# Kernel tuning notes

Hardware: AMD Instinct MI355X
Metric: run time of the kernel (lower is better)

## Reference

```python
import jax, jax.numpy as jnp
import numpy as np

EMBED_DIM = 128
HIDDEN_DIM = 512
NUM_LAYERS = 2
LATENT_DIM = 128
VOCAB = 2048
BATCH = 4096
NEG = -1.0e9  # matches torch masked fill value -1e9
TEMPERATURE = 1.0  # generate() skips the divide when temperature == 1.0


def _gru_cell(x, h, w_ih, w_hh, b_ih, b_hh):
    # PyTorch GRU cell, gate order (r, z, n)
    gi = x @ w_ih.T + b_ih          # [B, 3H]
    gh = h @ w_hh.T + b_hh          # [B, 3H]
    i_r, i_z, i_n = jnp.split(gi, 3, axis=-1)
    h_r, h_z, h_n = jnp.split(gh, 3, axis=-1)
    r = jax.nn.sigmoid(i_r + h_r)
    u = jax.nn.sigmoid(i_z + h_z)
    n = jnp.tanh(i_n + r * h_n)
    return (1.0 - u) * n + u * h


def setup_inputs() -> dict:
    key = jax.random.key(0)
    ks = jax.random.split(key, 16)

    def unif(k, shape, fan):
        bound = 1.0 / np.sqrt(fan)
        return jax.random.uniform(k, shape, jnp.float32, -bound, bound)

    embed = jax.random.normal(ks[0], (VOCAB, EMBED_DIM), jnp.float32)
    embed = embed.at[0].set(0.0)  # padding_idx = 0

    return dict(
        z=jax.random.normal(ks[1], (BATCH, LATENT_DIM), jnp.float32),
        embed=embed,
        w_lh=unif(ks[2], (NUM_LAYERS * HIDDEN_DIM, LATENT_DIM), LATENT_DIM),
        b_lh=unif(ks[3], (NUM_LAYERS * HIDDEN_DIM,), LATENT_DIM),
        w_ih0=unif(ks[4], (3 * HIDDEN_DIM, EMBED_DIM), HIDDEN_DIM),
        w_hh0=unif(ks[5], (3 * HIDDEN_DIM, HIDDEN_DIM), HIDDEN_DIM),
        b_ih0=unif(ks[6], (3 * HIDDEN_DIM,), HIDDEN_DIM),
        b_hh0=unif(ks[7], (3 * HIDDEN_DIM,), HIDDEN_DIM),
        w_ih1=unif(ks[8], (3 * HIDDEN_DIM, HIDDEN_DIM), HIDDEN_DIM),
        w_hh1=unif(ks[9], (3 * HIDDEN_DIM, HIDDEN_DIM), HIDDEN_DIM),
        b_ih1=unif(ks[10], (3 * HIDDEN_DIM,), HIDDEN_DIM),
        b_hh1=unif(ks[11], (3 * HIDDEN_DIM,), HIDDEN_DIM),
        w_out=unif(ks[12], (VOCAB, HIDDEN_DIM), HIDDEN_DIM),
        b_out=unif(ks[13], (VOCAB,), HIDDEN_DIM),
        bos_idx=1, eos_idx=2, pad_idx=0,
        max_len=64, top_k=40, min_generation_length=20,
    )


def reference(z, embed, w_lh, b_lh, w_ih0, w_hh0, b_ih0, b_hh0,
              w_ih1, w_hh1, b_ih1, b_hh1, w_out, b_out,
              bos_idx, eos_idx, pad_idx, max_len, top_k, min_generation_length):
    B = z.shape[0]
    V = w_out.shape[0]
    H = w_hh0.shape[1]
    eff_min = max(0, min(int(min_generation_length), max(0, max_len - 2)))

    # latent -> initial hidden state [L, B, H]
    h = jnp.tanh(z @ w_lh.T + b_lh).reshape(B, NUM_LAYERS, H).transpose(1, 0, 2)
    rows = jnp.arange(B)[:, None]

    def step(carry, t):
        h, cur, finished, key = carry
        key, sk = jax.random.split(key)
        x = embed[cur]                                   # [B, E]
        h0 = _gru_cell(x, h[0], w_ih0, w_hh0, b_ih0, b_hh0)
        h1 = _gru_cell(h0, h[1], w_ih1, w_hh1, b_ih1, b_hh1)
        logits = h1 @ w_out.T + b_out                    # [B, V]
        logits = logits.at[:, bos_idx].set(NEG).at[:, pad_idx].set(NEG)
        # block EOS until min_generation_length real tokens emitted
        logits = jnp.where((t - 1) < eff_min, logits.at[:, eos_idx].set(NEG), logits)
        if TEMPERATURE != 1.0:
            logits = logits / max(TEMPERATURE, 1e-6)
        if 0 < top_k < V:
            tv, ti = jax.lax.top_k(logits, top_k)
            logits = jnp.full_like(logits, NEG).at[rows, ti].set(tv)
        # multinomial over softmax(logits) == categorical on logits
        nxt = jax.random.categorical(sk, logits).astype(jnp.int32)
        nxt = jnp.where(finished, pad_idx, nxt)
        finished = finished | (nxt == eos_idx)
        return (jnp.stack([h0, h1]), nxt, finished, key), nxt

    init = (h,
            jnp.full((B,), bos_idx, jnp.int32),
            jnp.zeros((B,), dtype=bool),
            jax.random.key(1))
    _, toks = jax.lax.scan(step, init, jnp.arange(1, max_len))  # toks: [max_len-1, B]
    return jnp.concatenate(
        [jnp.full((B, 1), bos_idx, jnp.int32), toks.T.astype(jnp.int32)], axis=1)
```

## Files before the change

kernel.cpp:

```cpp
#include <hip/hip_runtime.h>
#include <cstdint>
#include <cstddef>

#ifndef PARTITIONABLE
#define PARTITIONABLE 1
#endif

namespace {
constexpr int kBatch  = 4096;
constexpr int kEmb    = 128;
constexpr int kHid    = 512;
constexpr int kVoc    = 2048;
constexpr int kMaxLen = 64;
constexpr int kTopK   = 40;
constexpr int kBos = 1, kEos = 2, kPad = 0;
constexpr int kEffMin = 20;
constexpr float kNeg  = -1.0e9f;
constexpr float kTiny = 1.17549435082228751e-38f;
}

typedef __bf16 bf16x8 __attribute__((ext_vector_type(8)));
typedef float  f32x4  __attribute__((ext_vector_type(4)));

__host__ __device__ inline void tf2x32(uint32_t k0, uint32_t k1,
                                       uint32_t x0, uint32_t x1,
                                       uint32_t& o0, uint32_t& o1) {
  uint32_t ks0 = k0, ks1 = k1, ks2 = k0 ^ k1 ^ 0x1BD11BDAu;
  x0 += ks0; x1 += ks1;
#define TFR(r) { x0 += x1; x1 = (x1 << (r)) | (x1 >> (32 - (r))); x1 ^= x0; }
  TFR(13) TFR(15) TFR(26) TFR(6)   x0 += ks1; x1 += ks2 + 1u;
  TFR(17) TFR(29) TFR(16) TFR(24)  x0 += ks2; x1 += ks0 + 2u;
  TFR(13) TFR(15) TFR(26) TFR(6)   x0 += ks0; x1 += ks1 + 3u;
  TFR(17) TFR(29) TFR(16) TFR(24)  x0 += ks1; x1 += ks2 + 4u;
  TFR(13) TFR(15) TFR(26) TFR(6)   x0 += ks2; x1 += ks0 + 5u;
#undef TFR
  o0 = x0; o1 = x1;
}

__device__ __forceinline__ float xla_tanh(float x) {
  float ax = fabsf(x);
  float xc = fminf(fmaxf(x, -9.0f), 9.0f);
  float x2 = __fmul_rn(xc, xc);
  float num = -2.76076847742355e-16f;
  num = __fadd_rn(__fmul_rn(x2, num), 2.00018790482477e-13f);
  num = __fadd_rn(__fmul_rn(x2, num), -8.60467152213735e-11f);
  num = __fadd_rn(__fmul_rn(x2, num), 5.12229709037114e-08f);
  num = __fadd_rn(__fmul_rn(x2, num), 1.48572235717979e-05f);
  num = __fadd_rn(__fmul_rn(x2, num), 6.37261928875436e-04f);
  num = __fadd_rn(__fmul_rn(x2, num), 4.89352455891786e-03f);
  num = __fmul_rn(xc, num);
  float den = 1.19825839466702e-06f;
  den = __fadd_rn(__fmul_rn(x2, den), 1.18534705686654e-04f);
  den = __fadd_rn(__fmul_rn(x2, den), 2.26843463243900e-03f);
  den = __fadd_rn(__fmul_rn(x2, den), 4.89352518554385e-03f);
  return (ax < 4.0e-04f) ? x : __fdiv_rn(num, den);
}

__device__ __forceinline__ float xla_sigmoid(float x) {
  return __fdiv_rn(1.0f, __fadd_rn(1.0f, expf(-x)));
}

__device__ __forceinline__ void gl_lds16(const void* g, void* l) {
  __builtin_amdgcn_global_load_lds(
      (const __attribute__((address_space(1))) void*)g,
      (__attribute__((address_space(3))) void*)l, 16, 0, 0);
}

__device__ __forceinline__ void split3(float a, __bf16& a0, __bf16& a1, __bf16& a2) {
  a0 = (__bf16)a;
  float r1 = __fsub_rn(a, (float)a0);
  a1 = (__bf16)r1;
  float r2 = __fsub_rn(r1, (float)a1);
  a2 = (__bf16)r2;
}

template <int ACT>
__global__ __launch_bounds__(256) void gemm2(
    const float* __restrict__ A0, const float* __restrict__ B0,
    const float* __restrict__ bias0, float* __restrict__ C0,
    const float* __restrict__ A1, const float* __restrict__ B1,
    const float* __restrict__ bias1, float* __restrict__ C1,
    int lda, int ldb, int ldc, int K) {
  __shared__ __attribute__((aligned(16))) float As[2][128 * 16];
  __shared__ __attribute__((aligned(16))) float Bs[2][16 * 128];

  const float* A    = blockIdx.z ? A1 : A0;
  const float* Bt   = blockIdx.z ? B1 : B0;
  const float* bias = blockIdx.z ? bias1 : bias0;
  float*       C    = blockIdx.z ? C1 : C0;

  const int tid = threadIdx.x;
  const int w = tid >> 6, l = tid & 63;
  const int bm = blockIdx.y * 128;
  const int bn = blockIdx.x * 128;
  const int tx = tid & 15, ty = tid >> 4;
  const int t3 = ty & 3;

  const int arow  = w * 16 + (l >> 2);
  const int agran = (l & 3) ^ ((l >> 2) & 3);
  const float* pA = A + (size_t)(bm + arow) * lda + agran * 4;
  const int bk = w * 2 + (l >> 5);
  const int bnc = (l & 31) * 4;
  const float* pB = Bt + (size_t)bk * ldb + bn + bnc;

  float acc[8][8];
#pragma unroll
  for (int i = 0; i < 8; ++i)
#pragma unroll
    for (int j = 0; j < 8; ++j) acc[i][j] = 0.0f;

  const int nt = K >> 4;
  gl_lds16(pA,            &As[0][w * 256]);
  gl_lds16(pA + 64 * lda, &As[0][(4 + w) * 256]);
  gl_lds16(pB,            &Bs[0][w * 256]);
  gl_lds16(pB + (size_t)8 * ldb, &Bs[0][(4 + w) * 256]);
  __syncthreads();

  for (int t = 0; t < nt; ++t) {
    const int cur = t & 1;
    if (t + 1 < nt) {
      const float* qA = pA + (t + 1) * 16;
      const float* qB = pB + (size_t)(t + 1) * 16 * ldb;
      gl_lds16(qA,            &As[cur ^ 1][w * 256]);
      gl_lds16(qA + 64 * lda, &As[cur ^ 1][(4 + w) * 256]);
      gl_lds16(qB,            &Bs[cur ^ 1][w * 256]);
      gl_lds16(qB + (size_t)8 * ldb, &Bs[cur ^ 1][(4 + w) * 256]);
    }
    const float* as = As[cur];
    const float* bs = Bs[cur];
#pragma unroll
    for (int g = 0; g < 4; ++g) {
      float4 bv0[4], bv1[4];
#pragma unroll
      for (int q = 0; q < 4; ++q) {
        bv0[q] = *(const float4*)&bs[(g * 4 + q) * 128 + tx * 4];
        bv1[q] = *(const float4*)&bs[(g * 4 + q) * 128 + 64 + tx * 4];
      }
#pragma unroll
      for (int ii = 0; ii < 8; ++ii) {
        float4 a = *(const float4*)&as[(ty + 16 * ii) * 16 + ((g ^ t3) * 4)];
        float ak[4] = {a.x, a.y, a.z, a.w};
#pragma unroll
        for (int q = 0; q < 4; ++q) {
          const float av_ = ak[q];
          const float4 b0 = bv0[q], b1 = bv1[q];
          acc[ii][0] += av_ * b0.x; acc[ii][1] += av_ * b0.y;
          acc[ii][2] += av_ * b0.z; acc[ii][3] += av_ * b0.w;
          acc[ii][4] += av_ * b1.x; acc[ii][5] += av_ * b1.y;
          acc[ii][6] += av_ * b1.z; acc[ii][7] += av_ * b1.w;
        }
      }
    }
    __syncthreads();
  }

  const int c0 = bn + tx * 4, c1 = bn + 64 + tx * 4;
  const float4 bs0 = *(const float4*)&bias[c0];
  const float4 bs1 = *(const float4*)&bias[c1];
#pragma unroll
  for (int ii = 0; ii < 8; ++ii) {
    const int r = bm + ty + 16 * ii;
    float4 o0, o1;
    o0.x = acc[ii][0] + bs0.x; o0.y = acc[ii][1] + bs0.y;
    o0.z = acc[ii][2] + bs0.z; o0.w = acc[ii][3] + bs0.w;
    o1.x = acc[ii][4] + bs1.x; o1.y = acc[ii][5] + bs1.y;
    o1.z = acc[ii][6] + bs1.z; o1.w = acc[ii][7] + bs1.w;
    if (ACT == 1) {
      o0.x = xla_tanh(o0.x); o0.y = xla_tanh(o0.y);
      o0.z = xla_tanh(o0.z); o0.w = xla_tanh(o0.w);
      o1.x = xla_tanh(o1.x); o1.y = xla_tanh(o1.y);
      o1.z = xla_tanh(o1.z); o1.w = xla_tanh(o1.w);
    }
    *(float4*)(C + (size_t)r * ldc + c0) = o0;
    *(float4*)(C + (size_t)r * ldc + c1) = o1;
  }
}

struct GemmArgs {
  const __bf16 *a0, *a1, *a2;
  const __bf16 *b0, *b1, *b2;
  const float* bias;
  float* c;
};

__global__ __launch_bounds__(256, 3) void gemm_mx3(
    GemmArgs g0, GemmArgs g1, int N) {
  __shared__ __attribute__((aligned(16))) __bf16 lds[6 * 4096];

  const GemmArgs g = blockIdx.z ? g1 : g0;
  const int tid = threadIdx.x;
  const int nwg = gridDim.x * gridDim.y;
  const int lin = blockIdx.y * gridDim.x + blockIdx.x;
  const int swz = (lin & 7) * (nwg >> 3) + (lin >> 3);
  const int bm = (swz / gridDim.x) * 128;
  const int bn = (swz % gridDim.x) * 128;
  const int lane = tid & 63;
  const int w  = tid >> 6;
  const int wm = w & 1;
  const int wn = w >> 1;
  const int l15 = lane & 15;
  const int kge = (lane >> 4) * 8;

  const int srow = tid >> 2;
  const int sge  = (tid & 3) * 8;
  const __bf16* tp[6];
  tp[0] = g.a0 + (size_t)(bm + srow) * 512 + sge;
  tp[1] = g.a1 + (size_t)(bm + srow) * 512 + sge;
  tp[2] = g.a2 + (size_t)(bm + srow) * 512 + sge;
  tp[3] = g.b0 + (size_t)(bn + srow) * 512 + sge;
  tp[4] = g.b1 + (size_t)(bn + srow) * 512 + sge;
  tp[5] = g.b2 + (size_t)(bn + srow) * 512 + sge;

  int aoff[4], boff[4];
#pragma unroll
  for (int i = 0; i < 4; ++i) {
    aoff[i] = (wm * 64 + i * 16 + l15) * 32 + kge;
    boff[i] = (wn * 64 + i * 16 + l15) * 32 + kge;
  }

  f32x4 acc[4][4] = {};

  for (int s = 0; s < 16; ++s) {
    const int k0 = s * 32;
#pragma unroll
    for (int p = 0; p < 6; ++p) {
      gl_lds16(tp[p] + k0,                    &lds[p * 4096 + w * 512]);
      gl_lds16(tp[p] + (size_t)64 * 512 + k0, &lds[p * 4096 + 2048 + w * 512]);
    }
    __syncthreads();

    bf16x8 Af[3][4];
#pragma unroll
    for (int mi = 0; mi < 4; ++mi) {
      Af[0][mi] = *(const bf16x8*)&lds[0 * 4096 + aoff[mi]];
      Af[1][mi] = *(const bf16x8*)&lds[1 * 4096 + aoff[mi]];
      Af[2][mi] = *(const bf16x8*)&lds[2 * 4096 + aoff[mi]];
    }
#pragma unroll
    for (int nj = 0; nj < 4; ++nj) {
      bf16x8 B0 = *(const bf16x8*)&lds[3 * 4096 + boff[nj]];
      bf16x8 B1 = *(const bf16x8*)&lds[4 * 4096 + boff[nj]];
      bf16x8 B2 = *(const bf16x8*)&lds[5 * 4096 + boff[nj]];
#pragma unroll
      for (int mi = 0; mi < 4; ++mi) {
        f32x4 c = acc[mi][nj];
        c = __builtin_amdgcn_mfma_f32_16x16x32_bf16(Af[2][mi], B2, c, 0, 0, 0);
        c = __builtin_amdgcn_mfma_f32_16x16x32_bf16(Af[2][mi], B1, c, 0, 0, 0);
        c = __builtin_amdgcn_mfma_f32_16x16x32_bf16(Af[1][mi], B2, c, 0, 0, 0);
        c = __builtin_amdgcn_mfma_f32_16x16x32_bf16(Af[2][mi], B0, c, 0, 0, 0);
        c = __builtin_amdgcn_mfma_f32_16x16x32_bf16(Af[1][mi], B1, c, 0, 0, 0);
        c = __builtin_amdgcn_mfma_f32_16x16x32_bf16(Af[0][mi], B2, c, 0, 0, 0);
        c = __builtin_amdgcn_mfma_f32_16x16x32_bf16(Af[1][mi], B0, c, 0, 0, 0);
        c = __builtin_amdgcn_mfma_f32_16x16x32_bf16(Af[0][mi], B1, c, 0, 0, 0);
        c = __builtin_amdgcn_mfma_f32_16x16x32_bf16(Af[0][mi], B0, c, 0, 0, 0);
        acc[mi][nj] = c;
      }
    }
    __syncthreads();
  }

#pragma unroll
  for (int mi = 0; mi < 4; ++mi) {
    const int row0 = bm + wm * 64 + mi * 16 + (lane >> 4) * 4;
#pragma unroll
    for (int nj = 0; nj < 4; ++nj) {
      const int col = bn + wn * 64 + nj * 16 + l15;
      const float bv = g.bias[col];
      f32x4 v = acc[mi][nj];
#pragma unroll
      for (int r = 0; r < 4; ++r)
        g.c[(size_t)(row0 + r) * N + col] = v[r] + bv;
    }
  }
}

__global__ __launch_bounds__(256, 2) void gemm_gru0(
    const __bf16* __restrict__ a0, const __bf16* __restrict__ a1,
    const __bf16* __restrict__ a2,
    const __bf16* __restrict__ wb0, const __bf16* __restrict__ wb1,
    const __bf16* __restrict__ wb2,
    const float* __restrict__ bias, const float* __restrict__ Eih0,
    const int* __restrict__ curTok,
    __bf16* __restrict__ q0, __bf16* __restrict__ q1,
    __bf16* __restrict__ q2) {
  __shared__ __attribute__((aligned(16))) __bf16 As[3][4096];
  __shared__ __attribute__((aligned(16))) __bf16 Bs[9][1024];

  const int tid = threadIdx.x;
  const int nwg = gridDim.x * gridDim.y;
  const int lin = blockIdx.y * gridDim.x + blockIdx.x;
  const int swz = (lin & 7) * (nwg >> 3) + (lin >> 3);
  const int bm = (swz / gridDim.x) * 128;
  const int bn = (swz % gridDim.x) * 32;
  const int lane = tid & 63;
  const int w  = tid >> 6;
  const int wm = w & 1;
  const int wn = w >> 1;
  const int l15 = lane & 15;
  const int kge = (lane >> 4) * 8;

  const int srow = tid >> 2;
  const int sge  = (tid & 3) * 8;
  const __bf16* tpA[3];
  tpA[0] = a0 + (size_t)(bm + srow) * 512 + sge;
  tpA[1] = a1 + (size_t)(bm + srow) * 512 + sge;
  tpA[2] = a2 + (size_t)(bm + srow) * 512 + sge;

  const int bcol = lane >> 2;
  const int bge  = (lane & 3) * 8;

  int aoff[4];
#pragma unroll
  for (int i = 0; i < 4; ++i)
    aoff[i] = (wm * 64 + i * 16 + l15) * 32 + kge;
  const int boff = (wn * 16 + l15) * 32 + kge;

  f32x4 acc[3][4] = {};

  for (int s = 0; s < 16; ++s) {
    const int k0 = s * 32;
#pragma unroll
    for (int p = 0; p < 3; ++p) {
      gl_lds16(tpA[p] + k0,                    &As[p][w * 512]);
      gl_lds16(tpA[p] + (size_t)64 * 512 + k0, &As[p][2048 + w * 512]);
    }
    for (int qq = w; qq < 9; qq += 4) {
      const int gg = qq / 3, pp = qq - gg * 3;
      const __bf16* wp = (pp == 0) ? wb0 : (pp == 1) ? wb1 : wb2;
      const __bf16* src =
          wp + (size_t)(gg * 512 + bn + bcol) * 512 + bge + k0;
      gl_lds16(src,                     &Bs[qq][0]);
      gl_lds16(src + (size_t)16 * 512,  &Bs[qq][512]);
    }
    __syncthreads();

    bf16x8 Af[3][4];
#pragma unroll
    for (int mi = 0; mi < 4; ++mi) {
      Af[0][mi] = *(const bf16x8*)&As[0][aoff[mi]];
      Af[1][mi] = *(const bf16x8*)&As[1][aoff[mi]];
      Af[2][mi] = *(const bf16x8*)&As[2][aoff[mi]];
    }
#pragma unroll
    for (int gg = 0; gg < 3; ++gg) {
      bf16x8 B0 = *(const bf16x8*)&Bs[gg * 3 + 0][boff];
      bf16x8 B1 = *(const bf16x8*)&Bs[gg * 3 + 1][boff];
      bf16x8 B2 = *(const bf16x8*)&Bs[gg * 3 + 2][boff];
#pragma unroll
      for (int mi = 0; mi < 4; ++mi) {
        f32x4 c = acc[gg][mi];
        c = __builtin_amdgcn_mfma_f32_16x16x32_bf16(Af[2][mi], B2, c, 0, 0, 0);
        c = __builtin_amdgcn_mfma_f32_16x16x32_bf16(Af[2][mi], B1, c, 0, 0, 0);
        c = __builtin_amdgcn_mfma_f32_16x16x32_bf16(Af[1][mi], B2, c, 0, 0, 0);
        c = __builtin_amdgcn_mfma_f32_16x16x32_bf16(Af[2][mi], B0, c, 0, 0, 0);
        c = __builtin_amdgcn_mfma_f32_16x16x32_bf16(Af[1][mi], B1, c, 0, 0, 0);
        c = __builtin_amdgcn_mfma_f32_16x16x32_bf16(Af[0][mi], B2, c, 0, 0, 0);
        c = __builtin_amdgcn_mfma_f32_16x16x32_bf16(Af[1][mi], B0, c, 0, 0, 0);
        c = __builtin_amdgcn_mfma_f32_16x16x32_bf16(Af[0][mi], B1, c, 0, 0, 0);
        c = __builtin_amdgcn_mfma_f32_16x16x32_bf16(Af[0][mi], B0, c, 0, 0, 0);
        acc[gg][mi] = c;
      }
    }
    __syncthreads();
  }

  const int col = bn + wn * 16 + l15;
  const float bvr = bias[col];
  const float bvz = bias[512 + col];
  const float bvn = bias[1024 + col];
#pragma unroll
  for (int mi = 0; mi < 4; ++mi) {
    const int row0 = bm + wm * 64 + mi * 16 + (lane >> 4) * 4;
#pragma unroll
    for (int rr = 0; rr < 4; ++rr) {
      const int row = row0 + rr;
      const int tok = curTok[row];
      const float* e = Eih0 + (size_t)tok * 1536;
      float gir = e[col], giz = e[512 + col], gin = e[1024 + col];
      float ghr = acc[0][mi][rr] + bvr;
      float ghz = acc[1][mi][rr] + bvz;
      float ghn = acc[2][mi][rr] + bvn;
      float r = xla_sigmoid(__fadd_rn(gir, ghr));
      float u = xla_sigmoid(__fadd_rn(giz, ghz));
      float n = xla_tanh(__fadd_rn(gin, __fmul_rn(r, ghn)));
      const size_t idx = (size_t)row * 512 + col;
      float hold = __fadd_rn(__fadd_rn((float)a0[idx], (float)a1[idx]),
                             (float)a2[idx]);
      float t1 = __fmul_rn(__fsub_rn(1.0f, u), n);
      float t2 = __fmul_rn(u, hold);
      float hnew = __fadd_rn(t1, t2);
      __bf16 s0, s1, s2;
      split3(hnew, s0, s1, s2);
      q0[idx] = s0; q1[idx] = s1; q2[idx] = s2;
    }
  }
}

__global__ __launch_bounds__(256) void k_split(
    const float* __restrict__ in, __bf16* __restrict__ p0,
    __bf16* __restrict__ p1, __bf16* __restrict__ p2, int total) {
  int i = blockIdx.x * 256 + threadIdx.x;
  if (i >= total) return;
  __bf16 a0, a1, a2;
  split3(in[i], a0, a1, a2);
  p0[i] = a0; p1[i] = a1; p2[i] = a2;
}

__global__ __launch_bounds__(256) void k_transpose(
    const float* __restrict__ in, float* __restrict__ out, int R, int C) {
  __shared__ float tile[32][33];
  int c0 = blockIdx.x * 32, r0 = blockIdx.y * 32;
  int x = threadIdx.x, y0 = threadIdx.y;
  for (int i = y0; i < 32; i += 8) {
    int r = r0 + i, c = c0 + x;
    tile[i][x] = (r < R && c < C) ? in[(size_t)r * C + c] : 0.0f;
  }
  __syncthreads();
  for (int i = y0; i < 32; i += 8) {
    int orow = c0 + i, oc = r0 + x;
    if (orow < C && oc < R) out[(size_t)orow * R + oc] = tile[x][i];
  }
}

__global__ __launch_bounds__(256) void k_gates(
    const float* __restrict__ gi_mat, const int* __restrict__ gi_rows,
    const float* __restrict__ gh,
    __bf16* __restrict__ p0, __bf16* __restrict__ p1, __bf16* __restrict__ p2) {
  int idx = blockIdx.x * 256 + threadIdx.x;
  int b = idx >> 9, j = idx & 511;
  int gr = gi_rows ? gi_rows[b] : b;
  const float* gi = gi_mat + (size_t)gr * 1536;
  const float* gp = gh + (size_t)b * 1536;
  float ir = gi[j], iz = gi[512 + j], in_ = gi[1024 + j];
  float hr = gp[j], hz = gp[512 + j], hn = gp[1024 + j];
  float r = xla_sigmoid(__fadd_rn(ir, hr));
  float u = xla_sigmoid(__fadd_rn(iz, hz));
  float n = xla_tanh(__fadd_rn(in_, __fmul_rn(r, hn)));
  float hold = __fadd_rn(__fadd_rn((float)p0[idx], (float)p1[idx]), (float)p2[idx]);
  float t1 = __fmul_rn(__fsub_rn(1.0f, u), n);
  float t2 = __fmul_rn(u, hold);
  float hnew = __fadd_rn(t1, t2);
  __bf16 a0, a1, a2;
  split3(hnew, a0, a1, a2);
  p0[idx] = a0; p1[idx] = a1; p2[idx] = a2;
}

__global__ __launch_bounds__(256) void k_sample(
    const float* __restrict__ logits, int* __restrict__ cur,
    int* __restrict__ finished, int* __restrict__ outTok,
    int t, uint32_t sk0, uint32_t sk1) {
  const int row = blockIdx.x;
  const int tid = threadIdx.x;
  __shared__ float sl[kVoc];
  __shared__ uint32_t skeys[kVoc];
  __shared__ int   redi[4];
  __shared__ float redf[4];
  __shared__ int   redix[4];

  const float* lp = logits + (size_t)row * kVoc;
  for (int c = tid; c < kVoc; c += 256) {
    float v = lp[c];
    if (c == kBos || c == kPad) v = kNeg;
    if (c == kEos && t < 1 + kEffMin) v = kNeg;
    sl[c] = v;
    uint32_t u = __float_as_uint(v);
    skeys[c] = u ^ ((u >> 31) ? 0xFFFFFFFFu : 0x80000000u);
  }
  __syncthreads();

  uint32_t prefix = 0u;
  for (int b = 31; b >= 0; --b) {
    uint32_t trial = prefix | (1u << b);
    int cnt = 0;
    for (int c = tid; c < kVoc; c += 256) cnt += (skeys[c] >= trial) ? 1 : 0;
#pragma unroll
    for (int off = 32; off; off >>= 1) cnt += __shfl_down(cnt, off, 64);
    __syncthreads();
    if ((tid & 63) == 0) redi[tid >> 6] = cnt;
    __syncthreads();
    int total = redi[0] + redi[1] + redi[2] + redi[3];
    if (total >= kTopK) prefix = trial;
  }

  float best = -3.4e38f; int bidx = kVoc;
  for (int c = tid; c < kVoc; c += 256) {
    if (skeys[c] >= prefix) {
      uint32_t idx = (uint32_t)row * (uint32_t)kVoc + (uint32_t)c;
      uint32_t w1, w2, bits;
#if PARTITIONABLE
      tf2x32(sk0, sk1, 0u, idx, w1, w2);
      bits = w1 ^ w2;
#else
      const uint32_t HH = (uint32_t)((uint64_t)kBatch * kVoc / 2);
      if (idx < HH) { tf2x32(sk0, sk1, idx, idx + HH, w1, w2); bits = w1; }
      else          { tf2x32(sk0, sk1, idx - HH, idx, w1, w2); bits = w2; }
#endif
      uint32_t fb = (bits >> 9) | 0x3f800000u;
      float uf = __fsub_rn(__uint_as_float(fb), 1.0f);
      if (uf == 0.0f) uf = kTiny;
      float g = -logf(-logf(uf));
      float tot = __fadd_rn(g, sl[c]);
      if (tot > best || (tot == best && c < bidx)) { best = tot; bidx = c; }
    }
  }
#pragma unroll
  for (int off = 32; off; off >>= 1) {
    float ov = __shfl_down(best, off, 64);
    int   oi = __shfl_down(bidx, off, 64);
    if (ov > best || (ov == best && oi < bidx)) { best = ov; bidx = oi; }
  }
  if ((tid & 63) == 0) { redf[tid >> 6] = best; redix[tid >> 6] = bidx; }
  __syncthreads();
  if (tid == 0) {
    for (int w = 1; w < 4; ++w) {
      if (redf[w] > best || (redf[w] == best && redix[w] < bidx)) {
        best = redf[w]; bidx = redix[w];
      }
    }
    int fin = finished[row];
    int nxt = fin ? kPad : bidx;
    outTok[(size_t)row * kMaxLen + t] = nxt;
    cur[row] = nxt;
    finished[row] = fin | (nxt == kEos);
  }
}

__global__ __launch_bounds__(256) void k_init(int* cur, int* finished, int* outTok) {
  int i = blockIdx.x * 256 + threadIdx.x;
  if (i < kBatch) {
    cur[i] = kBos;
    finished[i] = 0;
    outTok[(size_t)i * kMaxLen] = kBos;
  }
}

extern "C" void kernel_launch(void* const* d_in, const int* in_sizes, int n_in,
                              void* d_out, int out_size, void* d_ws, size_t ws_size,
                              hipStream_t stream) {
  (void)in_sizes; (void)n_in; (void)out_size; (void)ws_size;
  const float* z      = (const float*)d_in[0];
  const float* embed  = (const float*)d_in[1];
  const float* w_lh   = (const float*)d_in[2];
  const float* b_lh   = (const float*)d_in[3];
  const float* w_ih0  = (const float*)d_in[4];
  const float* w_hh0  = (const float*)d_in[5];
  const float* b_ih0  = (const float*)d_in[6];
  const float* b_hh0  = (const float*)d_in[7];
  const float* w_ih1  = (const float*)d_in[8];
  const float* w_hh1  = (const float*)d_in[9];
  const float* b_ih1  = (const float*)d_in[10];
  const float* b_hh1  = (const float*)d_in[11];
  const float* w_out  = (const float*)d_in[12];
  const float* b_out  = (const float*)d_in[13];
  int* out = (int*)d_out;

  char* base = (char*)d_ws;
  int* curTok   = (int*)base;
  int* finished = curTok + kBatch;
  __bf16* q = (__bf16*)(base + 32768);
  __bf16* whh0[3]; __bf16* wih1[3]; __bf16* whh1[3]; __bf16* wout[3];
  for (int i = 0; i < 3; ++i) { whh0[i] = q; q += (size_t)1536 * 512; }
  for (int i = 0; i < 3; ++i) { wih1[i] = q; q += (size_t)1536 * 512; }
  for (int i = 0; i < 3; ++i) { whh1[i] = q; q += (size_t)1536 * 512; }
  for (int i = 0; i < 3; ++i) { wout[i] = q; q += (size_t)2048 * 512; }
  __bf16* hs0A[3]; __bf16* hs1[3];
  for (int i = 0; i < 3; ++i) { hs0A[i] = q; q += (size_t)kBatch * kHid; }
  for (int i = 0; i < 3; ++i) { hs1[i] = q; q += (size_t)kBatch * kHid; }
  float* f = (float*)q;
  float* Eih0 = f; f += (size_t)kVoc * 1536;
  float* ghA  = f; f += (size_t)kBatch * 1536;
  float* gi1  = f; f += (size_t)kBatch * 1536;
  float* logits = ghA;
  float* wt_ih0 = ghA;
  float* wt_lh  = ghA + (size_t)128 * 1536;
  float* h0tmp  = gi1;
  float* h1tmp  = gi1 + (size_t)kBatch * kHid;
  __bf16* hs0B[3];
  { __bf16* hb = (__bf16*)f;
    for (int i = 0; i < 3; ++i) { hs0B[i] = hb; hb += (size_t)kBatch * kHid; } }

  dim3 blk(256);
  dim3 tblk(32, 8);

  k_transpose<<<dim3(4, 48), tblk, 0, stream>>>(w_ih0, wt_ih0, 1536, 128);
  k_transpose<<<dim3(4, 32), tblk, 0, stream>>>(w_lh,  wt_lh,  1024, 128);
  k_split<<<dim3(1536 * 512 / 256), blk, 0, stream>>>(w_hh0, whh0[0], whh0[1], whh0[2], 1536 * 512);
  k_split<<<dim3(1536 * 512 / 256), blk, 0, stream>>>(w_ih1, wih1[0], wih1[1], wih1[2], 1536 * 512);
  k_split<<<dim3(1536 * 512 / 256), blk, 0, stream>>>(w_hh1, whh1[0], whh1[1], whh1[2], 1536 * 512);
  k_split<<<dim3(2048 * 512 / 256), blk, 0, stream>>>(w_out, wout[0], wout[1], wout[2], 2048 * 512);

  gemm2<0><<<dim3(12, 16, 1), blk, 0, stream>>>(
      embed, wt_ih0, b_ih0, Eih0, embed, wt_ih0, b_ih0, Eih0,
      kEmb, 1536, 1536, kEmb);
  gemm2<1><<<dim3(4, 32, 2), blk, 0, stream>>>(
      z, wt_lh,       b_lh,       h0tmp,
      z, wt_lh + 512, b_lh + 512, h1tmp,
      kEmb, 1024, kHid, kEmb);
  k_split<<<dim3(kBatch * kHid / 256), blk, 0, stream>>>(h0tmp, hs0A[0], hs0A[1], hs0A[2], kBatch * kHid);
  k_split<<<dim3(kBatch * kHid / 256), blk, 0, stream>>>(h1tmp, hs1[0], hs1[1], hs1[2], kBatch * kHid);
  k_init<<<dim3((kBatch + 255) / 256), blk, 0, stream>>>(curTok, finished, out);

  uint32_t key0 = 0u, key1 = 1u;
  for (int t = 1; t < kMaxLen; ++t) {
    uint32_t nk0, nk1, s0, s1;
#if PARTITIONABLE
    tf2x32(key0, key1, 0u, 0u, nk0, nk1);
    tf2x32(key0, key1, 0u, 1u, s0, s1);
#else
    uint32_t a0, b0w, a1, b1w;
    tf2x32(key0, key1, 0u, 2u, a0, b0w);
    tf2x32(key0, key1, 1u, 3u, a1, b1w);
    nk0 = a0; nk1 = a1; s0 = b0w; s1 = b1w;
#endif
    __bf16** h0in  = (t & 1) ? hs0A : hs0B;
    __bf16** h0out = (t & 1) ? hs0B : hs0A;

    gemm_gru0<<<dim3(16, 32), blk, 0, stream>>>(
        h0in[0], h0in[1], h0in[2], whh0[0], whh0[1], whh0[2],
        b_hh0, Eih0, curTok, h0out[0], h0out[1], h0out[2]);

    GemmArgs gia{h0out[0], h0out[1], h0out[2], wih1[0], wih1[1], wih1[2], b_ih1, gi1};
    GemmArgs gha{hs1[0], hs1[1], hs1[2], whh1[0], whh1[1], whh1[2], b_hh1, ghA};
    gemm_mx3<<<dim3(12, 32, 2), blk, 0, stream>>>(gia, gha, 1536);
    k_gates<<<dim3(kBatch * kHid / 256), blk, 0, stream>>>(
        gi1, nullptr, ghA, hs1[0], hs1[1], hs1[2]);

    GemmArgs gla{hs1[0], hs1[1], hs1[2], wout[0], wout[1], wout[2], b_out, logits};
    gemm_mx3<<<dim3(16, 32, 1), blk, 0, stream>>>(gla, gla, 2048);
    k_sample<<<dim3(kBatch), blk, 0, stream>>>(logits, curTok, finished, out, t, s0, s1);

    key0 = nk0; key1 = nk1;
  }
}
```

Measured before the change: 18.38 ms.

## Fuse layer-1 GRU input/hidden GEMMs and gate update into one kernel

```diff
diff --git a/kernel.cpp b/kernel.cpp
--- a/kernel.cpp
+++ b/kernel.cpp
@@ -74,6 +74,29 @@
   a2 = (__bf16)r2;
 }
 
+__device__ __forceinline__ float gru_h(float gir, float giz, float gin,
+                                       float ghr, float ghz, float ghn,
+                                       float hold) {
+  float r = xla_sigmoid(__fadd_rn(gir, ghr));
+  float u = xla_sigmoid(__fadd_rn(giz, ghz));
+  float n = xla_tanh(__fadd_rn(gin, __fmul_rn(r, ghn)));
+  float t1 = __fmul_rn(__fsub_rn(1.0f, u), n);
+  float t2 = __fmul_rn(u, hold);
+  return __fadd_rn(t1, t2);
+}
+
+#define MFMA9(c, A0_, A1_, A2_, B0_, B1_, B2_) do {                          \
+    c = __builtin_amdgcn_mfma_f32_16x16x32_bf16(A2_, B2_, c, 0, 0, 0);       \
+    c = __builtin_amdgcn_mfma_f32_16x16x32_bf16(A2_, B1_, c, 0, 0, 0);       \
+    c = __builtin_amdgcn_mfma_f32_16x16x32_bf16(A1_, B2_, c, 0, 0, 0);       \
+    c = __builtin_amdgcn_mfma_f32_16x16x32_bf16(A2_, B0_, c, 0, 0, 0);       \
+    c = __builtin_amdgcn_mfma_f32_16x16x32_bf16(A1_, B1_, c, 0, 0, 0);       \
+    c = __builtin_amdgcn_mfma_f32_16x16x32_bf16(A0_, B2_, c, 0, 0, 0);       \
+    c = __builtin_amdgcn_mfma_f32_16x16x32_bf16(A1_, B0_, c, 0, 0, 0);       \
+    c = __builtin_amdgcn_mfma_f32_16x16x32_bf16(A0_, B1_, c, 0, 0, 0);       \
+    c = __builtin_amdgcn_mfma_f32_16x16x32_bf16(A0_, B0_, c, 0, 0, 0);       \
+  } while (0)
+
 template <int ACT>
 __global__ __launch_bounds__(256) void gemm2(
     const float* __restrict__ A0, const float* __restrict__ B0,
@@ -244,15 +267,7 @@
 #pragma unroll
       for (int mi = 0; mi < 4; ++mi) {
         f32x4 c = acc[mi][nj];
-        c = __builtin_amdgcn_mfma_f32_16x16x32_bf16(Af[2][mi], B2, c, 0, 0, 0);
-        c = __builtin_amdgcn_mfma_f32_16x16x32_bf16(Af[2][mi], B1, c, 0, 0, 0);
-        c = __builtin_amdgcn_mfma_f32_16x16x32_bf16(Af[1][mi], B2, c, 0, 0, 0);
-        c = __builtin_amdgcn_mfma_f32_16x16x32_bf16(Af[2][mi], B0, c, 0, 0, 0);
-        c = __builtin_amdgcn_mfma_f32_16x16x32_bf16(Af[1][mi], B1, c, 0, 0, 0);
-        c = __builtin_amdgcn_mfma_f32_16x16x32_bf16(Af[0][mi], B2, c, 0, 0, 0);
-        c = __builtin_amdgcn_mfma_f32_16x16x32_bf16(Af[1][mi], B0, c, 0, 0, 0);
-        c = __builtin_amdgcn_mfma_f32_16x16x32_bf16(Af[0][mi], B1, c, 0, 0, 0);
-        c = __builtin_amdgcn_mfma_f32_16x16x32_bf16(Af[0][mi], B0, c, 0, 0, 0);
+        MFMA9(c, Af[0][mi], Af[1][mi], Af[2][mi], B0, B1, B2);
         acc[mi][nj] = c;
       }
     }
@@ -349,15 +364,7 @@
 #pragma unroll
       for (int mi = 0; mi < 4; ++mi) {
         f32x4 c = acc[gg][mi];
-        c = __builtin_amdgcn_mfma_f32_16x16x32_bf16(Af[2][mi], B2, c, 0, 0, 0);
-        c = __builtin_amdgcn_mfma_f32_16x16x32_bf16(Af[2][mi], B1, c, 0, 0, 0);
-        c = __builtin_amdgcn_mfma_f32_16x16x32_bf16(Af[1][mi], B2, c, 0, 0, 0);
-        c = __builtin_amdgcn_mfma_f32_16x16x32_bf16(Af[2][mi], B0, c, 0, 0, 0);
-        c = __builtin_amdgcn_mfma_f32_16x16x32_bf16(Af[1][mi], B1, c, 0, 0, 0);
-        c = __builtin_amdgcn_mfma_f32_16x16x32_bf16(Af[0][mi], B2, c, 0, 0, 0);
-        c = __builtin_amdgcn_mfma_f32_16x16x32_bf16(Af[1][mi], B0, c, 0, 0, 0);
-        c = __builtin_amdgcn_mfma_f32_16x16x32_bf16(Af[0][mi], B1, c, 0, 0, 0);
-        c = __builtin_amdgcn_mfma_f32_16x16x32_bf16(Af[0][mi], B0, c, 0, 0, 0);
+        MFMA9(c, Af[0][mi], Af[1][mi], Af[2][mi], B0, B1, B2);
         acc[gg][mi] = c;
       }
     }
@@ -376,22 +383,141 @@
       const int row = row0 + rr;
       const int tok = curTok[row];
       const float* e = Eih0 + (size_t)tok * 1536;
-      float gir = e[col], giz = e[512 + col], gin = e[1024 + col];
-      float ghr = acc[0][mi][rr] + bvr;
-      float ghz = acc[1][mi][rr] + bvz;
-      float ghn = acc[2][mi][rr] + bvn;
-      float r = xla_sigmoid(__fadd_rn(gir, ghr));
-      float u = xla_sigmoid(__fadd_rn(giz, ghz));
-      float n = xla_tanh(__fadd_rn(gin, __fmul_rn(r, ghn)));
       const size_t idx = (size_t)row * 512 + col;
       float hold = __fadd_rn(__fadd_rn((float)a0[idx], (float)a1[idx]),
                              (float)a2[idx]);
-      float t1 = __fmul_rn(__fsub_rn(1.0f, u), n);
-      float t2 = __fmul_rn(u, hold);
-      float hnew = __fadd_rn(t1, t2);
+      float hnew = gru_h(e[col], e[512 + col], e[1024 + col],
+                         acc[0][mi][rr] + bvr, acc[1][mi][rr] + bvz,
+                         acc[2][mi][rr] + bvn, hold);
       __bf16 s0, s1, s2;
       split3(hnew, s0, s1, s2);
       q0[idx] = s0; q1[idx] = s1; q2[idx] = s2;
+    }
+  }
+}
+
+__global__ __launch_bounds__(256, 2) void gemm_gru1(
+    const __bf16* __restrict__ x0, const __bf16* __restrict__ x1,
+    const __bf16* __restrict__ x2,
+    const __bf16* __restrict__ wi0, const __bf16* __restrict__ wi1,
+    const __bf16* __restrict__ wi2,
+    const __bf16* __restrict__ wh0, const __bf16* __restrict__ wh1,
+    const __bf16* __restrict__ wh2,
+    const float* __restrict__ bias_i, const float* __restrict__ bias_h,
+    const __bf16* __restrict__ hi0, const __bf16* __restrict__ hi1,
+    const __bf16* __restrict__ hi2,
+    __bf16* __restrict__ ho0, __bf16* __restrict__ ho1,
+    __bf16* __restrict__ ho2) {
+  __shared__ __attribute__((aligned(16))) __bf16 As[6][2048];
+  __shared__ __attribute__((aligned(16))) __bf16 Bs[18][1024];
+
+  const int tid = threadIdx.x;
+  const int nwg = gridDim.x * gridDim.y;
+  const int lin = blockIdx.y * gridDim.x + blockIdx.x;
+  const int swz = (lin & 7) * (nwg >> 3) + (lin >> 3);
+  const int bm = (swz / gridDim.x) * 64;
+  const int bn = (swz % gridDim.x) * 32;
+  const int lane = tid & 63;
+  const int w  = tid >> 6;
+  const int wm = w & 1;
+  const int wn = w >> 1;
+  const int l15 = lane & 15;
+  const int kge = (lane >> 4) * 8;
+
+  const int srow = tid >> 2;
+  const int sge  = (tid & 3) * 8;
+  const __bf16* tpA[6];
+  tpA[0] = x0 + (size_t)(bm + srow) * 512 + sge;
+  tpA[1] = x1 + (size_t)(bm + srow) * 512 + sge;
+  tpA[2] = x2 + (size_t)(bm + srow) * 512 + sge;
+  tpA[3] = hi0 + (size_t)(bm + srow) * 512 + sge;
+  tpA[4] = hi1 + (size_t)(bm + srow) * 512 + sge;
+  tpA[5] = hi2 + (size_t)(bm + srow) * 512 + sge;
+
+  const int bcol = lane >> 2;
+  const int bge  = (lane & 3) * 8;
+
+  int aoff[2];
+#pragma unroll
+  for (int i = 0; i < 2; ++i)
+    aoff[i] = (wm * 32 + i * 16 + l15) * 32 + kge;
+  const int boff = (wn * 16 + l15) * 32 + kge;
+
+  f32x4 acci[3][2] = {};
+  f32x4 acch[3][2] = {};
+
+  const __bf16* wis[3] = {wi0, wi1, wi2};
+  const __bf16* whs[3] = {wh0, wh1, wh2};
+
+  for (int s = 0; s < 16; ++s) {
+    const int k0 = s * 32;
+#pragma unroll
+    for (int p = 0; p < 6; ++p)
+      gl_lds16(tpA[p] + k0, &As[p][w * 512]);
+    for (int qq = w; qq < 18; qq += 4) {
+      const int wset = qq / 9;
+      const int gg = (qq - wset * 9) / 3, pp = qq - wset * 9 - gg * 3;
+      const __bf16* wp = wset ? whs[pp] : wis[pp];
+      const __bf16* src = wp + (size_t)(gg * 512 + bn + bcol) * 512 + bge + k0;
+      gl_lds16(src,                    &Bs[qq][0]);
+      gl_lds16(src + (size_t)16 * 512, &Bs[qq][512]);
+    }
+    __syncthreads();
+
+    bf16x8 Xf[3][2], Hf[3][2];
+#pragma unroll
+    for (int mi = 0; mi < 2; ++mi) {
+      Xf[0][mi] = *(const bf16x8*)&As[0][aoff[mi]];
+      Xf[1][mi] = *(const bf16x8*)&As[1][aoff[mi]];
+      Xf[2][mi] = *(const bf16x8*)&As[2][aoff[mi]];
+      Hf[0][mi] = *(const bf16x8*)&As[3][aoff[mi]];
+      Hf[1][mi] = *(const bf16x8*)&As[4][aoff[mi]];
+      Hf[2][mi] = *(const bf16x8*)&As[5][aoff[mi]];
+    }
+#pragma unroll
+    for (int gg = 0; gg < 3; ++gg) {
+      bf16x8 Bi0 = *(const bf16x8*)&Bs[gg * 3 + 0][boff];
+      bf16x8 Bi1 = *(const bf16x8*)&Bs[gg * 3 + 1][boff];
+      bf16x8 Bi2 = *(const bf16x8*)&Bs[gg * 3 + 2][boff];
+      bf16x8 Bh0 = *(const bf16x8*)&Bs[9 + gg * 3 + 0][boff];
+      bf16x8 Bh1 = *(const bf16x8*)&Bs[9 + gg * 3 + 1][boff];
+      bf16x8 Bh2 = *(const bf16x8*)&Bs[9 + gg * 3 + 2][boff];
+#pragma unroll
+      for (int mi = 0; mi < 2; ++mi) {
+        f32x4 ci = acci[gg][mi];
+        MFMA9(ci, Xf[0][mi], Xf[1][mi], Xf[2][mi], Bi0, Bi1, Bi2);
+        acci[gg][mi] = ci;
+        f32x4 ch = acch[gg][mi];
+        MFMA9(ch, Hf[0][mi], Hf[1][mi], Hf[2][mi], Bh0, Bh1, Bh2);
+        acch[gg][mi] = ch;
+      }
+    }
+    __syncthreads();
+  }
+
+  const int col = bn + wn * 16 + l15;
+  const float bir = bias_i[col];
+  const float biz = bias_i[512 + col];
+  const float bin = bias_i[1024 + col];
+  const float bhr = bias_h[col];
+  const float bhz = bias_h[512 + col];
+  const float bhn = bias_h[1024 + col];
+#pragma unroll
+  for (int mi = 0; mi < 2; ++mi) {
+    const int row0 = bm + wm * 32 + mi * 16 + (lane >> 4) * 4;
+#pragma unroll
+    for (int rr = 0; rr < 4; ++rr) {
+      const int row = row0 + rr;
+      const size_t idx = (size_t)row * 512 + col;
+      float hold = __fadd_rn(__fadd_rn((float)hi0[idx], (float)hi1[idx]),
+                             (float)hi2[idx]);
+      float hnew = gru_h(acci[0][mi][rr] + bir, acci[1][mi][rr] + biz,
+                         acci[2][mi][rr] + bin,
+                         acch[0][mi][rr] + bhr, acch[1][mi][rr] + bhz,
+                         acch[2][mi][rr] + bhn, hold);
+      __bf16 s0, s1, s2;
+      split3(hnew, s0, s1, s2);
+      ho0[idx] = s0; ho1[idx] = s1; ho2[idx] = s2;
     }
   }
 }
@@ -420,29 +546,6 @@
     int orow = c0 + i, oc = r0 + x;
     if (orow < C && oc < R) out[(size_t)orow * R + oc] = tile[x][i];
   }
-}
-
-__global__ __launch_bounds__(256) void k_gates(
-    const float* __restrict__ gi_mat, const int* __restrict__ gi_rows,
-    const float* __restrict__ gh,
-    __bf16* __restrict__ p0, __bf16* __restrict__ p1, __bf16* __restrict__ p2) {
-  int idx = blockIdx.x * 256 + threadIdx.x;
-  int b = idx >> 9, j = idx & 511;
-  int gr = gi_rows ? gi_rows[b] : b;
-  const float* gi = gi_mat + (size_t)gr * 1536;
-  const float* gp = gh + (size_t)b * 1536;
-  float ir = gi[j], iz = gi[512 + j], in_ = gi[1024 + j];
-  float hr = gp[j], hz = gp[512 + j], hn = gp[1024 + j];
-  float r = xla_sigmoid(__fadd_rn(ir, hr));
-  float u = xla_sigmoid(__fadd_rn(iz, hz));
-  float n = xla_tanh(__fadd_rn(in_, __fmul_rn(r, hn)));
-  float hold = __fadd_rn(__fadd_rn((float)p0[idx], (float)p1[idx]), (float)p2[idx]);
-  float t1 = __fmul_rn(__fsub_rn(1.0f, u), n);
-  float t2 = __fmul_rn(u, hold);
-  float hnew = __fadd_rn(t1, t2);
-  __bf16 a0, a1, a2;
-  split3(hnew, a0, a1, a2);
-  p0[idx] = a0; p1[idx] = a1; p2[idx] = a2;
 }
 
 __global__ __launch_bounds__(256) void k_sample(
@@ -563,9 +666,9 @@
   for (int i = 0; i < 3; ++i) { wih1[i] = q; q += (size_t)1536 * 512; }
   for (int i = 0; i < 3; ++i) { whh1[i] = q; q += (size_t)1536 * 512; }
   for (int i = 0; i < 3; ++i) { wout[i] = q; q += (size_t)2048 * 512; }
-  __bf16* hs0A[3]; __bf16* hs1[3];
+  __bf16* hs0A[3]; __bf16* hs1A[3];
   for (int i = 0; i < 3; ++i) { hs0A[i] = q; q += (size_t)kBatch * kHid; }
-  for (int i = 0; i < 3; ++i) { hs1[i] = q; q += (size_t)kBatch * kHid; }
+  for (int i = 0; i < 3; ++i) { hs1A[i] = q; q += (size_t)kBatch * kHid; }
   float* f = (float*)q;
   float* Eih0 = f; f += (size_t)kVoc * 1536;
   float* ghA  = f; f += (size_t)kBatch * 1536;
@@ -578,6 +681,10 @@
   __bf16* hs0B[3];
   { __bf16* hb = (__bf16*)f;
     for (int i = 0; i < 3; ++i) { hs0B[i] = hb; hb += (size_t)kBatch * kHid; } }
+  __bf16* hs1B[3];
+  {
+    __bf16* hb = (__bf16*)(gi1 + (size_t)kBatch * kHid);
+    for (int i = 0; i < 3; ++i) { hs1B[i] = hb; hb += (size_t)kBatch * kHid; } }
 
   dim3 blk(256);
   dim3 tblk(32, 8);
@@ -597,7 +704,7 @@
       z, wt_lh + 512, b_lh + 512, h1tmp,
       kEmb, 1024, kHid, kEmb);
   k_split<<<dim3(kBatch * kHid / 256), blk, 0, stream>>>(h0tmp, hs0A[0], hs0A[1], hs0A[2], kBatch * kHid);
-  k_split<<<dim3(kBatch * kHid / 256), blk, 0, stream>>>(h1tmp, hs1[0], hs1[1], hs1[2], kBatch * kHid);
+  k_split<<<dim3(kBatch * kHid / 256), blk, 0, stream>>>(h1tmp, hs1A[0], hs1A[1], hs1A[2], kBatch * kHid);
   k_init<<<dim3((kBatch + 255) / 256), blk, 0, stream>>>(curTok, finished, out);
 
   uint32_t key0 = 0u, key1 = 1u;
@@ -614,18 +721,22 @@
 #endif
     __bf16** h0in  = (t & 1) ? hs0A : hs0B;
     __bf16** h0out = (t & 1) ? hs0B : hs0A;
+    __bf16** h1in  = (t & 1) ? hs1A : hs1B;
+    __bf16** h1out = (t & 1) ? hs1B : hs1A;
 
     gemm_gru0<<<dim3(16, 32), blk, 0, stream>>>(
         h0in[0], h0in[1], h0in[2], whh0[0], whh0[1], whh0[2],
         b_hh0, Eih0, curTok, h0out[0], h0out[1], h0out[2]);
 
-    GemmArgs gia{h0out[0], h0out[1], h0out[2], wih1[0], wih1[1], wih1[2], b_ih1, gi1};
-    GemmArgs gha{hs1[0], hs1[1], hs1[2], whh1[0], whh1[1], whh1[2], b_hh1, ghA};
-    gemm_mx3<<<dim3(12, 32, 2), blk, 0, stream>>>(gia, gha, 1536);
-    k_gates<<<dim3(kBatch * kHid / 256), blk, 0, stream>>>(
-        gi1, nullptr, ghA, hs1[0], hs1[1], hs1[2]);
-
-    GemmArgs gla{hs1[0], hs1[1], hs1[2], wout[0], wout[1], wout[2], b_out, logits};
+    gemm_gru1<<<dim3(16, 64), blk, 0, stream>>>(
+        h0out[0], h0out[1], h0out[2],
+        wih1[0], wih1[1], wih1[2],
+        whh1[0], whh1[1], whh1[2],
+        b_ih1, b_hh1,
+        h1in[0], h1in[1], h1in[2],
+        h1out[0], h1out[1], h1out[2]);
+
+    GemmArgs gla{h1out[0], h1out[1], h1out[2], wout[0], wout[1], wout[2], b_out, logits};
     gemm_mx3<<<dim3(16, 32, 1), blk, 0, stream>>>(gla, gla, 2048);
     k_sample<<<dim3(kBatch), blk, 0, stream>>>(logits, curTok, finished, out, t, s0, s1);
 
```

Result: slower. 19.81 ms (+7.8%).
